# Optimization experiments

Hardware: AMD Instinct MI355X
Metric: run time of the kernel (lower is better)

## Reference

```python
import jax, jax.numpy as jnp
import numpy as np

B, T, H = 1024, 512, 128
TIMESTEPS_PREDICT = 4


def setup_inputs() -> dict:
    key = jax.random.key(0)
    ks = jax.random.split(key, 7)
    s = 1.0 / np.sqrt(H)
    return {
        "x": jax.random.normal(ks[0], (B, T, 1), jnp.float32),
        "hidden": jnp.zeros((B, H), jnp.float32),
        "fc0_w": jax.random.normal(ks[1], (H, 1), jnp.float32) * s,
        "fc0_b": jax.random.normal(ks[2], (H,), jnp.float32) * 0.1,
        "fc_w": jax.random.normal(ks[3], (H, H), jnp.float32) * s,
        "fc_b": jax.random.normal(ks[4], (H,), jnp.float32) * 0.1,
        "dec_w": jax.random.normal(ks[5], (1, H), jnp.float32) * s,
        "dec_b": jax.random.normal(ks[6], (1,), jnp.float32) * 0.1,
    }


def _rnn(x, h, fc0_w, fc0_b, fc_w, fc_b):
    """Vanilla tanh RNN over time. x: (B, Tx, 1), h: (B, H) -> (ys (B, Tx, H), h)."""
    def step(h, xt):  # xt: (B, 1)
        h = jnp.tanh(xt @ fc0_w.T + fc0_b + h @ fc_w.T + fc_b)
        return h, h
    h, ys = jax.lax.scan(step, h, jnp.swapaxes(x, 0, 1))  # ys: (Tx, B, H)
    return jnp.swapaxes(ys, 0, 1), h


def reference(x, hidden, fc0_w, fc0_b, fc_w, fc_b, dec_w, dec_b):
    out, h = _rnn(x, hidden, fc0_w, fc0_b, fc_w, fc_b)  # (B, T, H)
    y = out @ dec_w.T + dec_b  # (B, T, 1)
    last = y[:, -1:, :]  # (B, 1, 1)
    for _ in range(TIMESTEPS_PREDICT):
        out_h, h = _rnn(last, h, fc0_w, fc0_b, fc_w, fc_b)
        last = out_h @ dec_w.T + dec_b
        y = jnp.concatenate([y, last], axis=1)
    return y  # (B, T + TIMESTEPS_PREDICT, 1)
```

## Files before the change

kernel.cpp:

```cpp
#include <hip/hip_runtime.h>
#include <hip/hip_bf16.h>


#define BB 1024
#define TT 512
#define HH 128
#define TOUT 516
#define BM 16
#define XSTR 513
#define YSTR 517
#define PQS 36
#define TWOLOG2E 2.885390082f

typedef __attribute__((ext_vector_type(8))) _Float16 f16x8;
typedef __attribute__((ext_vector_type(4))) float f32x4;

#define MFMA16(A_, B_, C_) __builtin_amdgcn_mfma_f32_16x16x32_f16(A_, B_, C_, 0, 0, 0)

__global__ void detect_dtype(const void* w, int* flag) {
    const int lane = threadIdx.x;
    const __hip_bfloat16* p = (const __hip_bfloat16*)w;
    const float v0 = __bfloat162float(p[lane]);
    const float v1 = __bfloat162float(p[64 + lane]);
    const bool bad = !(fabsf(v0) < 100.0f) || !(fabsf(v1) < 100.0f);
    const unsigned long long m = __ballot(bad);
    if (lane == 0) *flag = (__popcll(m) > 4) ? 1 : 0;
}

template <bool F32>
__device__ __forceinline__ float ldg(const void* p, int idx) {
    if (F32) return ((const float*)p)[idx];
    return __bfloat162float(((const __hip_bfloat16*)p)[idx]);
}

__device__ __forceinline__ float red32(const float* pqrow) {
    const f32x4* v = (const f32x4*)pqrow;
    const f32x4 s = ((v[0] + v[1]) + (v[2] + v[3])) + ((v[4] + v[5]) + (v[6] + v[7]));
    return (s[0] + s[1]) + (s[2] + s[3]);
}

#define STEP(T_, CUR_, WRITEY_, DOPQ_, READX_, TAILX_) do {                     \
    f16x8 bfrag[4];                                                             \
    _Pragma("unroll")                                                           \
    for (int kf = 0; kf < 4; ++kf)                                              \
        bfrag[kf] = *(const f16x8*)&hbuf[CUR_][n][((((kf << 2) | q) ^ n) & 15) << 3]; \
    float xnext = 0.0f;                                                         \
    if (READX_) xnext = xs[n][(T_) + 1];                                        \
    float xv;                                                                   \
    if (TAILX_) xv = red32(&pq[((T_) - 1) & 1][n][0]) + dbv;                    \
    else        xv = xpref;                                                     \
    f32x4 acc0, acc1;                                                           \
    _Pragma("unroll")                                                           \
    for (int r = 0; r < 4; ++r) acc0[r] = fmaf(xv, w0v[r], bsum[r]);            \
    acc1 = (f32x4){0.f, 0.f, 0.f, 0.f};                                         \
    acc0 = MFMA16(wa[0], bfrag[0], acc0);                                       \
    acc1 = MFMA16(wa[1], bfrag[1], acc1);                                       \
    acc0 = MFMA16(wa[2], bfrag[2], acc0);                                       \
    acc1 = MFMA16(wa[3], bfrag[3], acc1);                                       \
    if (isw7 && (WRITEY_)) {               \
        f32x4 aD0 = (f32x4){0.f, 0.f, 0.f, 0.f};                                \
        f32x4 aD1 = (f32x4){0.f, 0.f, 0.f, 0.f};                                \
        aD0 = MFMA16(wa_d[0], bfrag[0], aD0);                                   \
        aD1 = MFMA16(wa_d[1], bfrag[1], aD1);                                   \
        aD0 = MFMA16(wa_d[2], bfrag[2], aD0);                                   \
        aD1 = MFMA16(wa_d[3], bfrag[3], aD1);                                   \
        const float yp = aD0[0] + aD1[0] + dbv;                                 \
        if (q == 0) ybuf[n][(T_) - 1] = yp;                                     \
    }                                                                           \
    float zs[4], ex[4], rc[4], hv[4];                                           \
    _Pragma("unroll")                                                           \
    for (int r = 0; r < 4; ++r) zs[r] = acc0[r] + acc1[r];                      \
    _Pragma("unroll")                                                           \
    for (int r = 0; r < 4; ++r) ex[r] = __builtin_amdgcn_exp2f(zs[r]);          \
    _Pragma("unroll")                                                           \
    for (int r = 0; r < 4; ++r) rc[r] = __builtin_amdgcn_rcpf(ex[r] + 1.0f);    \
    _Pragma("unroll")                                                           \
    for (int r = 0; r < 4; ++r) hv[r] = fmaf(-2.0f, rc[r], 1.0f);               \
    float p = 0.0f;                                                             \
    if (DOPQ_) {                                                                \
        _Pragma("unroll")                                                       \
        for (int r = 0; r < 4; ++r) p = fmaf(decv[r], hv[r], p);                \
    }                                                                           \
    uint2 pk;                                                                   \
    pk.x = __builtin_bit_cast(unsigned, __builtin_amdgcn_cvt_pkrtz(hv[0], hv[1])); \
    pk.y = __builtin_bit_cast(unsigned, __builtin_amdgcn_cvt_pkrtz(hv[2], hv[3])); \
    *(uint2*)&hbuf[(CUR_) ^ 1][n][((((2 * wv + (q >> 1)) ^ n) & 15) << 3) + ((q & 1) << 2)] = pk; \
    if (DOPQ_) pq[(T_) & 1][n][wv * 4 + q] = p;                                 \
    if (READX_) xpref = xnext;                                                  \
    __syncthreads();                                                            \
} while (0)

template <bool F32>
__device__ void rnn_body(const void* __restrict__ xg, const void* __restrict__ h0,
                         const void* __restrict__ w0, const void* __restrict__ b0,
                         const void* __restrict__ W,  const void* __restrict__ bw,
                         const void* __restrict__ dw, const void* __restrict__ db,
                         void* __restrict__ out,
                         float (*xs)[XSTR], float (*ybuf)[YSTR],
                         _Float16 (*hbuf)[BM][HH], float (*pq)[BM][PQS])
{
    const int tid  = threadIdx.x;
    const int lane = tid & 63;
    const int wv   = tid >> 6;
    const int q    = lane >> 4;
    const int n    = lane & 15;
    const int row0 = blockIdx.x * BM;
    const bool isw7 = (wv == 7);

    for (int idx = tid; idx < BM * TT; idx += 512) {
        const int rr = idx >> 9, t2 = idx & (TT - 1);
        xs[rr][t2] = ldg<F32>(xg, (row0 + rr) * TT + t2);
    }
    for (int idx = tid; idx < BM * HH; idx += 512) {
        const int rr = idx >> 7, ii = idx & (HH - 1);
        const int po = ((((ii >> 3) ^ rr) & 15) << 3) + (ii & 7);
        hbuf[0][rr][po] = (_Float16)ldg<F32>(h0, (row0 + rr) * HH + ii);
    }

    f16x8 wa[4];
    {
        const int ia = wv * 16 + n;
        #pragma unroll
        for (int kf = 0; kf < 4; ++kf) {
            const int kb = kf * 32 + q * 8;
            f16x8 fr;
            #pragma unroll
            for (int j = 0; j < 8; ++j)
                fr[j] = (_Float16)(TWOLOG2E * ldg<F32>(W, ia * HH + kb + j));
            wa[kf] = fr;
        }
    }
    f16x8 wa_d[4] = {};
    if (isw7) {
        #pragma unroll
        for (int kf = 0; kf < 4; ++kf) {
            const int kb = kf * 32 + q * 8;
            f16x8 fr = {};
            if (n == 0) {
                #pragma unroll
                for (int j = 0; j < 8; ++j) fr[j] = (_Float16)ldg<F32>(dw, kb + j);
            }
            wa_d[kf] = fr;
        }
    }
    float bsum[4], w0v[4], decv[4];
    #pragma unroll
    for (int r = 0; r < 4; ++r) {
        const int ic = wv * 16 + q * 4 + r;
        bsum[r] = TWOLOG2E * (ldg<F32>(b0, ic) + ldg<F32>(bw, ic));
        w0v[r]  = TWOLOG2E * ldg<F32>(w0, ic);
        decv[r] = ldg<F32>(dw, ic);
    }
    const float dbv = ldg<F32>(db, 0);

    __syncthreads();

    float xpref = xs[n][0];

    STEP(0, 0, false, false, true, false);

    #pragma unroll 1
    for (int t = 1; t < 511; t += 2) {
        STEP(t,     1, true, false, true, false);
        STEP(t + 1, 0, true, false, true, false);
    }

    STEP(511, 1, true, true, false, false);

    #pragma unroll 1
    for (int t = 512; t < 516; ++t) {
        STEP(t, t & 1, true, true, false, true);
    }

    if (isw7 && q == 0)
        ybuf[n][TOUT - 1] = red32(&pq[(TOUT - 1) & 1][n][0]) + dbv;
    __syncthreads();

    for (int rr = 0; rr < BM; ++rr)
        for (int t2 = tid; t2 < TOUT; t2 += 512) {
            const int o = (row0 + rr) * TOUT + t2;
            const float y = ybuf[rr][t2];
            if (F32) ((float*)out)[o] = y;
            else     ((__hip_bfloat16*)out)[o] = __float2bfloat16(y);
        }
}

__global__ __launch_bounds__(512, 2)
void rnn_mfma(const void* __restrict__ xg, const void* __restrict__ h0,
              const void* __restrict__ w0, const void* __restrict__ b0,
              const void* __restrict__ W,  const void* __restrict__ bw,
              const void* __restrict__ dw, const void* __restrict__ db,
              void* __restrict__ out, const int* __restrict__ flag)
{
    __shared__ float xs[BM][XSTR];
    __shared__ float ybuf[BM][YSTR];
    __shared__ __align__(16) _Float16 hbuf[2][BM][HH];
    __shared__ __align__(16) float pq[2][BM][PQS];

    const int f = *(volatile const int*)flag;
    if (f) rnn_body<true >(xg, h0, w0, b0, W, bw, dw, db, out, xs, ybuf, hbuf, pq);
    else   rnn_body<false>(xg, h0, w0, b0, W, bw, dw, db, out, xs, ybuf, hbuf, pq);
}

extern "C" void kernel_launch(void* const* d_in, const int* in_sizes, int n_in,
                              void* d_out, int out_size, void* d_ws, size_t ws_size,
                              hipStream_t stream) {
    int* flag = (int*)d_ws;
    detect_dtype<<<1, 64, 0, stream>>>(d_in[4], flag);
    rnn_mfma<<<BB / BM, 512, 0, stream>>>(d_in[0], d_in[1], d_in[2], d_in[3],
                                          d_in[4], d_in[5], d_in[6], d_in[7],
                                          d_out, flag);
}
```

Before: 215.0 us.

## Process 32 batch rows per block with interleaved MFMA chains and direct output stores

Doubles the rows per block from 16 to 32, so each wave runs two independent MFMA chains per timestep on the same weight fragments. This gives more instruction-level parallelism in the latency-bound recurrence and halves the number of barriers per row. The decoder output is split between waves 6 and 7 and written straight to global memory each step, so the shared y buffer and the final copy loop are gone. Only 32 blocks now run across the device, which risks idle CUs, and the per-step scattered global stores may add latency.

```diff
diff --git a/kernel.cpp b/kernel.cpp
--- a/kernel.cpp
+++ b/kernel.cpp
@@ -6,9 +6,8 @@
 #define TT 512
 #define HH 128
 #define TOUT 516
-#define BM 16
+#define BM 32
 #define XSTR 513
-#define YSTR 517
 #define PQS 36
 #define TWOLOG2E 2.885390082f
 
@@ -33,6 +32,12 @@
     return __bfloat162float(((const __hip_bfloat16*)p)[idx]);
 }
 
+template <bool F32>
+__device__ __forceinline__ void stg(void* p, int idx, float v) {
+    if (F32) ((float*)p)[idx] = v;
+    else     ((__hip_bfloat16*)p)[idx] = __float2bfloat16(v);
+}
+
 __device__ __forceinline__ float red32(const float* pqrow) {
     const f32x4* v = (const f32x4*)pqrow;
     const f32x4 s = ((v[0] + v[1]) + (v[2] + v[3])) + ((v[4] + v[5]) + (v[6] + v[7]));
@@ -40,53 +45,89 @@
 }
 
 #define STEP(T_, CUR_, WRITEY_, DOPQ_, READX_, TAILX_) do {                     \
-    f16x8 bfrag[4];                                                             \
-    _Pragma("unroll")                                                           \
-    for (int kf = 0; kf < 4; ++kf)                                              \
-        bfrag[kf] = *(const f16x8*)&hbuf[CUR_][n][((((kf << 2) | q) ^ n) & 15) << 3]; \
-    float xnext = 0.0f;                                                         \
-    if (READX_) xnext = xs[n][(T_) + 1];                                        \
-    float xv;                                                                   \
-    if (TAILX_) xv = red32(&pq[((T_) - 1) & 1][n][0]) + dbv;                    \
-    else        xv = xpref;                                                     \
-    f32x4 acc0, acc1;                                                           \
-    _Pragma("unroll")                                                           \
-    for (int r = 0; r < 4; ++r) acc0[r] = fmaf(xv, w0v[r], bsum[r]);            \
-    acc1 = (f32x4){0.f, 0.f, 0.f, 0.f};                                         \
-    acc0 = MFMA16(wa[0], bfrag[0], acc0);                                       \
-    acc1 = MFMA16(wa[1], bfrag[1], acc1);                                       \
-    acc0 = MFMA16(wa[2], bfrag[2], acc0);                                       \
-    acc1 = MFMA16(wa[3], bfrag[3], acc1);                                       \
-    if (isw7 && (WRITEY_)) {               \
-        f32x4 aD0 = (f32x4){0.f, 0.f, 0.f, 0.f};                                \
-        f32x4 aD1 = (f32x4){0.f, 0.f, 0.f, 0.f};                                \
-        aD0 = MFMA16(wa_d[0], bfrag[0], aD0);                                   \
-        aD1 = MFMA16(wa_d[1], bfrag[1], aD1);                                   \
-        aD0 = MFMA16(wa_d[2], bfrag[2], aD0);                                   \
-        aD1 = MFMA16(wa_d[3], bfrag[3], aD1);                                   \
-        const float yp = aD0[0] + aD1[0] + dbv;                                 \
-        if (q == 0) ybuf[n][(T_) - 1] = yp;                                     \
-    }                                                                           \
-    float zs[4], ex[4], rc[4], hv[4];                                           \
-    _Pragma("unroll")                                                           \
-    for (int r = 0; r < 4; ++r) zs[r] = acc0[r] + acc1[r];                      \
-    _Pragma("unroll")                                                           \
-    for (int r = 0; r < 4; ++r) ex[r] = __builtin_amdgcn_exp2f(zs[r]);          \
-    _Pragma("unroll")                                                           \
-    for (int r = 0; r < 4; ++r) rc[r] = __builtin_amdgcn_rcpf(ex[r] + 1.0f);    \
-    _Pragma("unroll")                                                           \
-    for (int r = 0; r < 4; ++r) hv[r] = fmaf(-2.0f, rc[r], 1.0f);               \
-    float p = 0.0f;                                                             \
+    f16x8 bfragA[4], bfragB[4];                                                 \
+    _Pragma("unroll")                                                           \
+    for (int kf = 0; kf < 4; ++kf) {                                            \
+        const int co = ((((kf << 2) | q) ^ n) & 15) << 3;                       \
+        bfragA[kf] = *(const f16x8*)&hbuf[CUR_][n][co];                         \
+        bfragB[kf] = *(const f16x8*)&hbuf[CUR_][16 + n][co];                    \
+    }                                                                           \
+    float xnA = 0.0f, xnB = 0.0f;                                               \
+    if (READX_) { xnA = xs[n][(T_) + 1]; xnB = xs[16 + n][(T_) + 1]; }          \
+    float xvA, xvB;                                                             \
+    if (TAILX_) { xvA = red32(&pq[((T_) - 1) & 1][n][0]) + dbv;                 \
+                  xvB = red32(&pq[((T_) - 1) & 1][16 + n][0]) + dbv; }          \
+    else        { xvA = xprefA; xvB = xprefB; }                                 \
+    f32x4 a0A, a1A, a0B, a1B;                                                   \
+    _Pragma("unroll")                                                           \
+    for (int r = 0; r < 4; ++r) { a0A[r] = fmaf(xvA, w0v[r], bsum[r]);          \
+                                  a0B[r] = fmaf(xvB, w0v[r], bsum[r]); }        \
+    a1A = (f32x4){0.f, 0.f, 0.f, 0.f};                                          \
+    a1B = (f32x4){0.f, 0.f, 0.f, 0.f};                                          \
+    a0A = MFMA16(wa[0], bfragA[0], a0A);                                        \
+    a0B = MFMA16(wa[0], bfragB[0], a0B);                                        \
+    a1A = MFMA16(wa[1], bfragA[1], a1A);                                        \
+    a1B = MFMA16(wa[1], bfragB[1], a1B);                                        \
+    a0A = MFMA16(wa[2], bfragA[2], a0A);                                        \
+    a0B = MFMA16(wa[2], bfragB[2], a0B);                                        \
+    a1A = MFMA16(wa[3], bfragA[3], a1A);                                        \
+    a1B = MFMA16(wa[3], bfragB[3], a1B);                                        \
+    if (WRITEY_) {                                                              \
+        if (isw7) {                   \
+            f32x4 dA0 = (f32x4){0.f, 0.f, 0.f, 0.f};                            \
+            f32x4 dA1 = (f32x4){0.f, 0.f, 0.f, 0.f};                            \
+            dA0 = MFMA16(wa_d[0], bfragA[0], dA0);                              \
+            dA1 = MFMA16(wa_d[1], bfragA[1], dA1);                              \
+            dA0 = MFMA16(wa_d[2], bfragA[2], dA0);                              \
+            dA1 = MFMA16(wa_d[3], bfragA[3], dA1);                              \
+            if (q == 0)                                                         \
+                stg<F32>(out, (row0 + n) * TOUT + (T_) - 1,                     \
+                         dA0[0] + dA1[0] + dbv);                                \
+        }                                                                       \
+        if (isw6) {                                             \
+            f32x4 dB0 = (f32x4){0.f, 0.f, 0.f, 0.f};                            \
+            f32x4 dB1 = (f32x4){0.f, 0.f, 0.f, 0.f};                            \
+            dB0 = MFMA16(wa_d[0], bfragB[0], dB0);                              \
+            dB1 = MFMA16(wa_d[1], bfragB[1], dB1);                              \
+            dB0 = MFMA16(wa_d[2], bfragB[2], dB0);                              \
+            dB1 = MFMA16(wa_d[3], bfragB[3], dB1);                              \
+            if (q == 0)                                                         \
+                stg<F32>(out, (row0 + 16 + n) * TOUT + (T_) - 1,                \
+                         dB0[0] + dB1[0] + dbv);                                \
+        }                                                                       \
+    }                                                                           \
+    float zsA[4], zsB[4], exA[4], exB[4], rcA[4], rcB[4], hvA[4], hvB[4];       \
+    _Pragma("unroll")                                                           \
+    for (int r = 0; r < 4; ++r) { zsA[r] = a0A[r] + a1A[r];                     \
+                                  zsB[r] = a0B[r] + a1B[r]; }                   \
+    _Pragma("unroll")                                                           \
+    for (int r = 0; r < 4; ++r) { exA[r] = __builtin_amdgcn_exp2f(zsA[r]);      \
+                                  exB[r] = __builtin_amdgcn_exp2f(zsB[r]); }    \
+    _Pragma("unroll")                                                           \
+    for (int r = 0; r < 4; ++r) { rcA[r] = __builtin_amdgcn_rcpf(exA[r] + 1.0f);\
+                                  rcB[r] = __builtin_amdgcn_rcpf(exB[r] + 1.0f);}\
+    _Pragma("unroll")                                                           \
+    for (int r = 0; r < 4; ++r) { hvA[r] = fmaf(-2.0f, rcA[r], 1.0f);           \
+                                  hvB[r] = fmaf(-2.0f, rcB[r], 1.0f); }         \
+    float pA = 0.0f, pB = 0.0f;                                                 \
     if (DOPQ_) {                                                                \
         _Pragma("unroll")                                                       \
-        for (int r = 0; r < 4; ++r) p = fmaf(decv[r], hv[r], p);                \
-    }                                                                           \
-    uint2 pk;                                                                   \
-    pk.x = __builtin_bit_cast(unsigned, __builtin_amdgcn_cvt_pkrtz(hv[0], hv[1])); \
-    pk.y = __builtin_bit_cast(unsigned, __builtin_amdgcn_cvt_pkrtz(hv[2], hv[3])); \
-    *(uint2*)&hbuf[(CUR_) ^ 1][n][((((2 * wv + (q >> 1)) ^ n) & 15) << 3) + ((q & 1) << 2)] = pk; \
-    if (DOPQ_) pq[(T_) & 1][n][wv * 4 + q] = p;                                 \
-    if (READX_) xpref = xnext;                                                  \
+        for (int r = 0; r < 4; ++r) { pA = fmaf(decv[r], hvA[r], pA);           \
+                                      pB = fmaf(decv[r], hvB[r], pB); }         \
+    }                                                                           \
+    uint2 pkA, pkB;                                                             \
+    pkA.x = __builtin_bit_cast(unsigned, __builtin_amdgcn_cvt_pkrtz(hvA[0], hvA[1])); \
+    pkA.y = __builtin_bit_cast(unsigned, __builtin_amdgcn_cvt_pkrtz(hvA[2], hvA[3])); \
+    pkB.x = __builtin_bit_cast(unsigned, __builtin_amdgcn_cvt_pkrtz(hvB[0], hvB[1])); \
+    pkB.y = __builtin_bit_cast(unsigned, __builtin_amdgcn_cvt_pkrtz(hvB[2], hvB[3])); \
+    {                                                                           \
+        const int wo = ((((2 * wv + (q >> 1)) ^ n) & 15) << 3) + ((q & 1) << 2);\
+        *(uint2*)&hbuf[(CUR_) ^ 1][n][wo]      = pkA;                           \
+        *(uint2*)&hbuf[(CUR_) ^ 1][16 + n][wo] = pkB;                           \
+    }                                                                           \
+    if (DOPQ_) { pq[(T_) & 1][n][wv * 4 + q]      = pA;                         \
+                 pq[(T_) & 1][16 + n][wv * 4 + q] = pB; }                       \
+    if (READX_) { xprefA = xnA; xprefB = xnB; }                                 \
     __syncthreads();                                                            \
 } while (0)
 
@@ -96,8 +137,8 @@
                          const void* __restrict__ W,  const void* __restrict__ bw,
                          const void* __restrict__ dw, const void* __restrict__ db,
                          void* __restrict__ out,
-                         float (*xs)[XSTR], float (*ybuf)[YSTR],
-                         _Float16 (*hbuf)[BM][HH], float (*pq)[BM][PQS])
+                         float (*xs)[XSTR], _Float16 (*hbuf)[BM][HH],
+                         float (*pq)[BM][PQS])
 {
     const int tid  = threadIdx.x;
     const int lane = tid & 63;
@@ -106,6 +147,7 @@
     const int n    = lane & 15;
     const int row0 = blockIdx.x * BM;
     const bool isw7 = (wv == 7);
+    const bool isw6 = (wv == 6);
 
     for (int idx = tid; idx < BM * TT; idx += 512) {
         const int rr = idx >> 9, t2 = idx & (TT - 1);
@@ -131,7 +173,7 @@
         }
     }
     f16x8 wa_d[4] = {};
-    if (isw7) {
+    if (wv >= 6) {
         #pragma unroll
         for (int kf = 0; kf < 4; ++kf) {
             const int kb = kf * 32 + q * 8;
@@ -155,7 +197,8 @@
 
     __syncthreads();
 
-    float xpref = xs[n][0];
+    float xprefA = xs[n][0];
+    float xprefB = xs[16 + n][0];
 
     STEP(0, 0, false, false, true, false);
 
@@ -173,16 +216,9 @@
     }
 
     if (isw7 && q == 0)
-        ybuf[n][TOUT - 1] = red32(&pq[(TOUT - 1) & 1][n][0]) + dbv;
-    __syncthreads();
-
-    for (int rr = 0; rr < BM; ++rr)
-        for (int t2 = tid; t2 < TOUT; t2 += 512) {
-            const int o = (row0 + rr) * TOUT + t2;
-            const float y = ybuf[rr][t2];
-            if (F32) ((float*)out)[o] = y;
-            else     ((__hip_bfloat16*)out)[o] = __float2bfloat16(y);
-        }
+        stg<F32>(out, (row0 + n) * TOUT + TOUT - 1, red32(&pq[1][n][0]) + dbv);
+    if (isw6 && q == 0)
+        stg<F32>(out, (row0 + 16 + n) * TOUT + TOUT - 1, red32(&pq[1][16 + n][0]) + dbv);
 }
 
 __global__ __launch_bounds__(512, 2)
@@ -193,13 +229,12 @@
               void* __restrict__ out, const int* __restrict__ flag)
 {
     __shared__ float xs[BM][XSTR];
-    __shared__ float ybuf[BM][YSTR];
     __shared__ __align__(16) _Float16 hbuf[2][BM][HH];
     __shared__ __align__(16) float pq[2][BM][PQS];
 
     const int f = *(volatile const int*)flag;
-    if (f) rnn_body<true >(xg, h0, w0, b0, W, bw, dw, db, out, xs, ybuf, hbuf, pq);
-    else   rnn_body<false>(xg, h0, w0, b0, W, bw, dw, db, out, xs, ybuf, hbuf, pq);
+    if (f) rnn_body<true >(xg, h0, w0, b0, W, bw, dw, db, out, xs, hbuf, pq);
+    else   rnn_body<false>(xg, h0, w0, b0, W, bw, dw, db, out, xs, hbuf, pq);
 }
 
 extern "C" void kernel_launch(void* const* d_in, const int* in_sizes, int n_in,
```

Result: slower. 305.5 us (+42.1%).

## Halve block to 4 waves, each computing two hidden tiles; write outputs directly

Applied to the files above, without the earlier changes.

Each block now uses 256 threads (4 waves). Each wave computes 32 hidden units using two interleaved MFMA chains, where before it computed 16, and the partial-product reduction shrinks to 16 entries. The shared y buffer and the final copy-out loop are removed, and the decoder output is stored straight to global memory at every step. Fewer waves means a cheaper per-step barrier and more independent MFMA work per wave. The trade-offs are twice the weight registers per wave and scattered small global stores inside the recurrence.

```diff
diff --git a/kernel.cpp b/kernel.cpp
--- a/kernel.cpp
+++ b/kernel.cpp
@@ -8,8 +8,7 @@
 #define TOUT 516
 #define BM 16
 #define XSTR 513
-#define YSTR 517
-#define PQS 36
+#define PQS 20
 #define TWOLOG2E 2.885390082f
 
 typedef __attribute__((ext_vector_type(8))) _Float16 f16x8;
@@ -33,9 +32,15 @@
     return __bfloat162float(((const __hip_bfloat16*)p)[idx]);
 }
 
-__device__ __forceinline__ float red32(const float* pqrow) {
+template <bool F32>
+__device__ __forceinline__ void stg(void* p, int idx, float v) {
+    if (F32) ((float*)p)[idx] = v;
+    else     ((__hip_bfloat16*)p)[idx] = __float2bfloat16(v);
+}
+
+__device__ __forceinline__ float red16(const float* pqrow) {
     const f32x4* v = (const f32x4*)pqrow;
-    const f32x4 s = ((v[0] + v[1]) + (v[2] + v[3])) + ((v[4] + v[5]) + (v[6] + v[7]));
+    const f32x4 s = (v[0] + v[1]) + (v[2] + v[3]);
     return (s[0] + s[1]) + (s[2] + s[3]);
 }
 
@@ -47,44 +52,63 @@
     float xnext = 0.0f;                                                         \
     if (READX_) xnext = xs[n][(T_) + 1];                                        \
     float xv;                                                                   \
-    if (TAILX_) xv = red32(&pq[((T_) - 1) & 1][n][0]) + dbv;                    \
+    if (TAILX_) xv = red16(&pq[((T_) - 1) & 1][n][0]) + dbv;                    \
     else        xv = xpref;                                                     \
-    f32x4 acc0, acc1;                                                           \
-    _Pragma("unroll")                                                           \
-    for (int r = 0; r < 4; ++r) acc0[r] = fmaf(xv, w0v[r], bsum[r]);            \
-    acc1 = (f32x4){0.f, 0.f, 0.f, 0.f};                                         \
-    acc0 = MFMA16(wa[0], bfrag[0], acc0);                                       \
-    acc1 = MFMA16(wa[1], bfrag[1], acc1);                                       \
-    acc0 = MFMA16(wa[2], bfrag[2], acc0);                                       \
-    acc1 = MFMA16(wa[3], bfrag[3], acc1);                                       \
-    if (isw7 && (WRITEY_)) {               \
-        f32x4 aD0 = (f32x4){0.f, 0.f, 0.f, 0.f};                                \
-        f32x4 aD1 = (f32x4){0.f, 0.f, 0.f, 0.f};                                \
-        aD0 = MFMA16(wa_d[0], bfrag[0], aD0);                                   \
-        aD1 = MFMA16(wa_d[1], bfrag[1], aD1);                                   \
-        aD0 = MFMA16(wa_d[2], bfrag[2], aD0);                                   \
-        aD1 = MFMA16(wa_d[3], bfrag[3], aD1);                                   \
-        const float yp = aD0[0] + aD1[0] + dbv;                                 \
-        if (q == 0) ybuf[n][(T_) - 1] = yp;                                     \
+    f32x4 a00, a01, a10, a11;                                                   \
+    _Pragma("unroll")                                                           \
+    for (int r = 0; r < 4; ++r) { a00[r] = fmaf(xv, w0v0[r], bsum0[r]);         \
+                                  a10[r] = fmaf(xv, w0v1[r], bsum1[r]); }       \
+    a01 = (f32x4){0.f, 0.f, 0.f, 0.f};                                          \
+    a11 = (f32x4){0.f, 0.f, 0.f, 0.f};                                          \
+    a00 = MFMA16(wa0[0], bfrag[0], a00);                                        \
+    a10 = MFMA16(wa1[0], bfrag[0], a10);                                        \
+    a01 = MFMA16(wa0[1], bfrag[1], a01);                                        \
+    a11 = MFMA16(wa1[1], bfrag[1], a11);                                        \
+    a00 = MFMA16(wa0[2], bfrag[2], a00);                                        \
+    a10 = MFMA16(wa1[2], bfrag[2], a10);                                        \
+    a01 = MFMA16(wa0[3], bfrag[3], a01);                                        \
+    a11 = MFMA16(wa1[3], bfrag[3], a11);                                        \
+    if (isw3 && (WRITEY_)) {               \
+        f32x4 dA0 = (f32x4){0.f, 0.f, 0.f, 0.f};                                \
+        f32x4 dA1 = (f32x4){0.f, 0.f, 0.f, 0.f};                                \
+        dA0 = MFMA16(wa_d[0], bfrag[0], dA0);                                   \
+        dA1 = MFMA16(wa_d[1], bfrag[1], dA1);                                   \
+        dA0 = MFMA16(wa_d[2], bfrag[2], dA0);                                   \
+        dA1 = MFMA16(wa_d[3], bfrag[3], dA1);                                   \
+        if (q == 0)                                                             \
+            stg<F32>(out, (row0 + n) * TOUT + (T_) - 1, dA0[0] + dA1[0] + dbv); \
     }                                                                           \
-    float zs[4], ex[4], rc[4], hv[4];                                           \
-    _Pragma("unroll")                                                           \
-    for (int r = 0; r < 4; ++r) zs[r] = acc0[r] + acc1[r];                      \
-    _Pragma("unroll")                                                           \
-    for (int r = 0; r < 4; ++r) ex[r] = __builtin_amdgcn_exp2f(zs[r]);          \
-    _Pragma("unroll")                                                           \
-    for (int r = 0; r < 4; ++r) rc[r] = __builtin_amdgcn_rcpf(ex[r] + 1.0f);    \
-    _Pragma("unroll")                                                           \
-    for (int r = 0; r < 4; ++r) hv[r] = fmaf(-2.0f, rc[r], 1.0f);               \
+    float zs0[4], zs1[4], ex0[4], ex1[4], rc0[4], rc1[4], hv0[4], hv1[4];       \
+    _Pragma("unroll")                                                           \
+    for (int r = 0; r < 4; ++r) { zs0[r] = a00[r] + a01[r];                     \
+                                  zs1[r] = a10[r] + a11[r]; }                   \
+    _Pragma("unroll")                                                           \
+    for (int r = 0; r < 4; ++r) { ex0[r] = __builtin_amdgcn_exp2f(zs0[r]);      \
+                                  ex1[r] = __builtin_amdgcn_exp2f(zs1[r]); }    \
+    _Pragma("unroll")                                                           \
+    for (int r = 0; r < 4; ++r) { rc0[r] = __builtin_amdgcn_rcpf(ex0[r] + 1.0f);\
+                                  rc1[r] = __builtin_amdgcn_rcpf(ex1[r] + 1.0f);}\
+    _Pragma("unroll")                                                           \
+    for (int r = 0; r < 4; ++r) { hv0[r] = fmaf(-2.0f, rc0[r], 1.0f);           \
+                                  hv1[r] = fmaf(-2.0f, rc1[r], 1.0f); }         \
     float p = 0.0f;                                                             \
     if (DOPQ_) {                                                                \
         _Pragma("unroll")                                                       \
-        for (int r = 0; r < 4; ++r) p = fmaf(decv[r], hv[r], p);                \
+        for (int r = 0; r < 4; ++r) { p = fmaf(decv0[r], hv0[r], p);            \
+                                      p = fmaf(decv1[r], hv1[r], p); }          \
     }                                                                           \
-    uint2 pk;                                                                   \
-    pk.x = __builtin_bit_cast(unsigned, __builtin_amdgcn_cvt_pkrtz(hv[0], hv[1])); \
-    pk.y = __builtin_bit_cast(unsigned, __builtin_amdgcn_cvt_pkrtz(hv[2], hv[3])); \
-    *(uint2*)&hbuf[(CUR_) ^ 1][n][((((2 * wv + (q >> 1)) ^ n) & 15) << 3) + ((q & 1) << 2)] = pk; \
+    uint2 pk0, pk1;                                                             \
+    pk0.x = __builtin_bit_cast(unsigned, __builtin_amdgcn_cvt_pkrtz(hv0[0], hv0[1])); \
+    pk0.y = __builtin_bit_cast(unsigned, __builtin_amdgcn_cvt_pkrtz(hv0[2], hv0[3])); \
+    pk1.x = __builtin_bit_cast(unsigned, __builtin_amdgcn_cvt_pkrtz(hv1[0], hv1[1])); \
+    pk1.y = __builtin_bit_cast(unsigned, __builtin_amdgcn_cvt_pkrtz(hv1[2], hv1[3])); \
+    {                   \
+        const int lo = ((q & 1) << 2);                                          \
+        const int c0 = ((((4 * wv) | (q >> 1)) ^ n) & 15) << 3;                 \
+        const int c1 = ((((4 * wv + 2) | (q >> 1)) ^ n) & 15) << 3;             \
+        *(uint2*)&hbuf[(CUR_) ^ 1][n][c0 + lo] = pk0;                           \
+        *(uint2*)&hbuf[(CUR_) ^ 1][n][c1 + lo] = pk1;                           \
+    }                                                                           \
     if (DOPQ_) pq[(T_) & 1][n][wv * 4 + q] = p;                                 \
     if (READX_) xpref = xnext;                                                  \
     __syncthreads();                                                            \
@@ -96,8 +120,8 @@
                          const void* __restrict__ W,  const void* __restrict__ bw,
                          const void* __restrict__ dw, const void* __restrict__ db,
                          void* __restrict__ out,
-                         float (*xs)[XSTR], float (*ybuf)[YSTR],
-                         _Float16 (*hbuf)[BM][HH], float (*pq)[BM][PQS])
+                         float (*xs)[XSTR], _Float16 (*hbuf)[BM][HH],
+                         float (*pq)[BM][PQS])
 {
     const int tid  = threadIdx.x;
     const int lane = tid & 63;
@@ -105,33 +129,37 @@
     const int q    = lane >> 4;
     const int n    = lane & 15;
     const int row0 = blockIdx.x * BM;
-    const bool isw7 = (wv == 7);
-
-    for (int idx = tid; idx < BM * TT; idx += 512) {
+    const bool isw3 = (wv == 3);
+
+    for (int idx = tid; idx < BM * TT; idx += 256) {
         const int rr = idx >> 9, t2 = idx & (TT - 1);
         xs[rr][t2] = ldg<F32>(xg, (row0 + rr) * TT + t2);
     }
-    for (int idx = tid; idx < BM * HH; idx += 512) {
+    for (int idx = tid; idx < BM * HH; idx += 256) {
         const int rr = idx >> 7, ii = idx & (HH - 1);
         const int po = ((((ii >> 3) ^ rr) & 15) << 3) + (ii & 7);
         hbuf[0][rr][po] = (_Float16)ldg<F32>(h0, (row0 + rr) * HH + ii);
     }
 
-    f16x8 wa[4];
+    f16x8 wa0[4], wa1[4];
     {
-        const int ia = wv * 16 + n;
+        const int ia0 = 32 * wv + n;
+        const int ia1 = 32 * wv + 16 + n;
         #pragma unroll
         for (int kf = 0; kf < 4; ++kf) {
             const int kb = kf * 32 + q * 8;
-            f16x8 fr;
+            f16x8 fr0, fr1;
             #pragma unroll
-            for (int j = 0; j < 8; ++j)
-                fr[j] = (_Float16)(TWOLOG2E * ldg<F32>(W, ia * HH + kb + j));
-            wa[kf] = fr;
+            for (int j = 0; j < 8; ++j) {
+                fr0[j] = (_Float16)(TWOLOG2E * ldg<F32>(W, ia0 * HH + kb + j));
+                fr1[j] = (_Float16)(TWOLOG2E * ldg<F32>(W, ia1 * HH + kb + j));
+            }
+            wa0[kf] = fr0;
+            wa1[kf] = fr1;
         }
     }
     f16x8 wa_d[4] = {};
-    if (isw7) {
+    if (isw3) {
         #pragma unroll
         for (int kf = 0; kf < 4; ++kf) {
             const int kb = kf * 32 + q * 8;
@@ -143,13 +171,17 @@
             wa_d[kf] = fr;
         }
     }
-    float bsum[4], w0v[4], decv[4];
+    float bsum0[4], w0v0[4], decv0[4], bsum1[4], w0v1[4], decv1[4];
     #pragma unroll
     for (int r = 0; r < 4; ++r) {
-        const int ic = wv * 16 + q * 4 + r;
-        bsum[r] = TWOLOG2E * (ldg<F32>(b0, ic) + ldg<F32>(bw, ic));
-        w0v[r]  = TWOLOG2E * ldg<F32>(w0, ic);
-        decv[r] = ldg<F32>(dw, ic);
+        const int ic0 = 32 * wv + q * 4 + r;
+        const int ic1 = ic0 + 16;
+        bsum0[r] = TWOLOG2E * (ldg<F32>(b0, ic0) + ldg<F32>(bw, ic0));
+        bsum1[r] = TWOLOG2E * (ldg<F32>(b0, ic1) + ldg<F32>(bw, ic1));
+        w0v0[r]  = TWOLOG2E * ldg<F32>(w0, ic0);
+        w0v1[r]  = TWOLOG2E * ldg<F32>(w0, ic1);
+        decv0[r] = ldg<F32>(dw, ic0);
+        decv1[r] = ldg<F32>(dw, ic1);
     }
     const float dbv = ldg<F32>(db, 0);
 
@@ -172,20 +204,11 @@
         STEP(t, t & 1, true, true, false, true);
     }
 
-    if (isw7 && q == 0)
-        ybuf[n][TOUT - 1] = red32(&pq[(TOUT - 1) & 1][n][0]) + dbv;
-    __syncthreads();
-
-    for (int rr = 0; rr < BM; ++rr)
-        for (int t2 = tid; t2 < TOUT; t2 += 512) {
-            const int o = (row0 + rr) * TOUT + t2;
-            const float y = ybuf[rr][t2];
-            if (F32) ((float*)out)[o] = y;
-            else     ((__hip_bfloat16*)out)[o] = __float2bfloat16(y);
-        }
-}
-
-__global__ __launch_bounds__(512, 2)
+    if (isw3 && q == 0)
+        stg<F32>(out, (row0 + n) * TOUT + TOUT - 1, red16(&pq[1][n][0]) + dbv);
+}
+
+__global__ __launch_bounds__(256, 1)
 void rnn_mfma(const void* __restrict__ xg, const void* __restrict__ h0,
               const void* __restrict__ w0, const void* __restrict__ b0,
               const void* __restrict__ W,  const void* __restrict__ bw,
@@ -193,13 +216,12 @@
               void* __restrict__ out, const int* __restrict__ flag)
 {
     __shared__ float xs[BM][XSTR];
-    __shared__ float ybuf[BM][YSTR];
     __shared__ __align__(16) _Float16 hbuf[2][BM][HH];
     __shared__ __align__(16) float pq[2][BM][PQS];
 
     const int f = *(volatile const int*)flag;
-    if (f) rnn_body<true >(xg, h0, w0, b0, W, bw, dw, db, out, xs, ybuf, hbuf, pq);
-    else   rnn_body<false>(xg, h0, w0, b0, W, bw, dw, db, out, xs, ybuf, hbuf, pq);
+    if (f) rnn_body<true >(xg, h0, w0, b0, W, bw, dw, db, out, xs, hbuf, pq);
+    else   rnn_body<false>(xg, h0, w0, b0, W, bw, dw, db, out, xs, hbuf, pq);
 }
 
 extern "C" void kernel_launch(void* const* d_in, const int* in_sizes, int n_in,
@@ -207,7 +229,7 @@
                               hipStream_t stream) {
     int* flag = (int*)d_ws;
     detect_dtype<<<1, 64, 0, stream>>>(d_in[4], flag);
-    rnn_mfma<<<BB / BM, 512, 0, stream>>>(d_in[0], d_in[1], d_in[2], d_in[3],
+    rnn_mfma<<<BB / BM, 256, 0, stream>>>(d_in[0], d_in[1], d_in[2], d_in[3],
                                           d_in[4], d_in[5], d_in[6], d_in[7],
                                           d_out, flag);
 }
```

Result: slower. 274.0 us (+27.4%).

## Defer decoder MFMA one step, write outputs directly, vectorize x prefetch

Applied to the files above, without the earlier changes.

The decoder projection for each step now runs at the start of the next step on the bfrag values still held in registers. This takes it off the critical path between the recurrence MFMAs and the tanh. Outputs go straight to global memory instead of being staged in an LDS ybuf and copied out at the end, which frees shared memory and removes the final copy loop. The x inputs are prefetched as float4 every four steps, the loop is unrolled by four, and launch bounds change to one block per SIMD group. The risks are scattered, uncoalesced global stores from a single wave and different occupancy.

```diff
diff --git a/kernel.cpp b/kernel.cpp
--- a/kernel.cpp
+++ b/kernel.cpp
@@ -7,8 +7,7 @@
 #define HH 128
 #define TOUT 516
 #define BM 16
-#define XSTR 513
-#define YSTR 517
+#define XSTR 516
 #define PQS 36
 #define TWOLOG2E 2.885390082f
 
@@ -33,22 +32,42 @@
     return __bfloat162float(((const __hip_bfloat16*)p)[idx]);
 }
 
+template <bool F32>
+__device__ __forceinline__ void stg(void* p, int idx, float v) {
+    if (F32) ((float*)p)[idx] = v;
+    else     ((__hip_bfloat16*)p)[idx] = __float2bfloat16(v);
+}
+
 __device__ __forceinline__ float red32(const float* pqrow) {
     const f32x4* v = (const f32x4*)pqrow;
     const f32x4 s = ((v[0] + v[1]) + (v[2] + v[3])) + ((v[4] + v[5]) + (v[6] + v[7]));
     return (s[0] + s[1]) + (s[2] + s[3]);
 }
 
-#define STEP(T_, CUR_, WRITEY_, DOPQ_, READX_, TAILX_) do {                     \
-    f16x8 bfrag[4];                                                             \
+#define STEP(T_, CUR_, DODEC_, DOPQ_, XSEL_, PFX_) do {                         \
+    if (isw7 && (DODEC_)) {          \
+        f32x4 dA0 = (f32x4){0.f, 0.f, 0.f, 0.f};                                \
+        f32x4 dA1 = (f32x4){0.f, 0.f, 0.f, 0.f};                                \
+        dA0 = MFMA16(wa_d[0], bfrag[0], dA0);                                   \
+        dA1 = MFMA16(wa_d[1], bfrag[1], dA1);                                   \
+        dA0 = MFMA16(wa_d[2], bfrag[2], dA0);                                   \
+        dA1 = MFMA16(wa_d[3], bfrag[3], dA1);                                   \
+        if (q == 0)                                                             \
+            stg<F32>(out, (row0 + n) * TOUT + (T_) - 2, dA0[0] + dA1[0] + dbv); \
+    }                                                                           \
     _Pragma("unroll")                                                           \
     for (int kf = 0; kf < 4; ++kf)                                              \
         bfrag[kf] = *(const f16x8*)&hbuf[CUR_][n][((((kf << 2) | q) ^ n) & 15) << 3]; \
-    float xnext = 0.0f;                                                         \
-    if (READX_) xnext = xs[n][(T_) + 1];                                        \
     float xv;                                                                   \
-    if (TAILX_) xv = red32(&pq[((T_) - 1) & 1][n][0]) + dbv;                    \
-    else        xv = xpref;                                                     \
+    if ((XSEL_) < 0) {                                                          \
+        xv = red32(&pq[((T_) - 1) & 1][n][0]) + dbv;                            \
+    } else {                                                                    \
+        if ((XSEL_) == 0) {                                                     \
+            xcur = xnxt;                                                        \
+            if (PFX_) xnxt = *(const f32x4*)&xs[n][(T_) + 4];                   \
+        }                                                                       \
+        xv = xcur[(XSEL_) & 3];                                                 \
+    }                                                                           \
     f32x4 acc0, acc1;                                                           \
     _Pragma("unroll")                                                           \
     for (int r = 0; r < 4; ++r) acc0[r] = fmaf(xv, w0v[r], bsum[r]);            \
@@ -57,16 +76,6 @@
     acc1 = MFMA16(wa[1], bfrag[1], acc1);                                       \
     acc0 = MFMA16(wa[2], bfrag[2], acc0);                                       \
     acc1 = MFMA16(wa[3], bfrag[3], acc1);                                       \
-    if (isw7 && (WRITEY_)) {               \
-        f32x4 aD0 = (f32x4){0.f, 0.f, 0.f, 0.f};                                \
-        f32x4 aD1 = (f32x4){0.f, 0.f, 0.f, 0.f};                                \
-        aD0 = MFMA16(wa_d[0], bfrag[0], aD0);                                   \
-        aD1 = MFMA16(wa_d[1], bfrag[1], aD1);                                   \
-        aD0 = MFMA16(wa_d[2], bfrag[2], aD0);                                   \
-        aD1 = MFMA16(wa_d[3], bfrag[3], aD1);                                   \
-        const float yp = aD0[0] + aD1[0] + dbv;                                 \
-        if (q == 0) ybuf[n][(T_) - 1] = yp;                                     \
-    }                                                                           \
     float zs[4], ex[4], rc[4], hv[4];                                           \
     _Pragma("unroll")                                                           \
     for (int r = 0; r < 4; ++r) zs[r] = acc0[r] + acc1[r];                      \
@@ -86,7 +95,6 @@
     pk.y = __builtin_bit_cast(unsigned, __builtin_amdgcn_cvt_pkrtz(hv[2], hv[3])); \
     *(uint2*)&hbuf[(CUR_) ^ 1][n][((((2 * wv + (q >> 1)) ^ n) & 15) << 3) + ((q & 1) << 2)] = pk; \
     if (DOPQ_) pq[(T_) & 1][n][wv * 4 + q] = p;                                 \
-    if (READX_) xpref = xnext;                                                  \
     __syncthreads();                                                            \
 } while (0)
 
@@ -96,8 +104,8 @@
                          const void* __restrict__ W,  const void* __restrict__ bw,
                          const void* __restrict__ dw, const void* __restrict__ db,
                          void* __restrict__ out,
-                         float (*xs)[XSTR], float (*ybuf)[YSTR],
-                         _Float16 (*hbuf)[BM][HH], float (*pq)[BM][PQS])
+                         float (*xs)[XSTR], _Float16 (*hbuf)[BM][HH],
+                         float (*pq)[BM][PQS])
 {
     const int tid  = threadIdx.x;
     const int lane = tid & 63;
@@ -155,37 +163,48 @@
 
     __syncthreads();
 
-    float xpref = xs[n][0];
-
-    STEP(0, 0, false, false, true, false);
+    f16x8 bfrag[4];
+    f32x4 xcur, xnxt;
+    xnxt = *(const f32x4*)&xs[n][0];
+
+    STEP(0, 0, false, false, 0, true);
+    STEP(1, 1, false, false, 1, false);
+    STEP(2, 0, true,  false, 2, false);
+    STEP(3, 1, true,  false, 3, false);
 
     #pragma unroll 1
-    for (int t = 1; t < 511; t += 2) {
-        STEP(t,     1, true, false, true, false);
-        STEP(t + 1, 0, true, false, true, false);
-    }
-
-    STEP(511, 1, true, true, false, false);
-
-    #pragma unroll 1
-    for (int t = 512; t < 516; ++t) {
-        STEP(t, t & 1, true, true, false, true);
-    }
-
-    if (isw7 && q == 0)
-        ybuf[n][TOUT - 1] = red32(&pq[(TOUT - 1) & 1][n][0]) + dbv;
-    __syncthreads();
-
-    for (int rr = 0; rr < BM; ++rr)
-        for (int t2 = tid; t2 < TOUT; t2 += 512) {
-            const int o = (row0 + rr) * TOUT + t2;
-            const float y = ybuf[rr][t2];
-            if (F32) ((float*)out)[o] = y;
-            else     ((__hip_bfloat16*)out)[o] = __float2bfloat16(y);
+    for (int t = 4; t < 508; t += 4) {
+        STEP(t,     0, true, false, 0, true);
+        STEP(t + 1, 1, true, false, 1, false);
+        STEP(t + 2, 0, true, false, 2, false);
+        STEP(t + 3, 1, true, false, 3, false);
+    }
+
+    STEP(508, 0, true, false, 0, false);
+    STEP(509, 1, true, false, 1, false);
+    STEP(510, 0, true, false, 2, false);
+    STEP(511, 1, true, true,  3, false);
+
+    STEP(512, 0, true, true, -1, false);
+    STEP(513, 1, true, true, -1, false);
+    STEP(514, 0, true, true, -1, false);
+    STEP(515, 1, true, true, -1, false);
+
+    if (isw7) {
+        f32x4 dA0 = (f32x4){0.f, 0.f, 0.f, 0.f};
+        f32x4 dA1 = (f32x4){0.f, 0.f, 0.f, 0.f};
+        dA0 = MFMA16(wa_d[0], bfrag[0], dA0);
+        dA1 = MFMA16(wa_d[1], bfrag[1], dA1);
+        dA0 = MFMA16(wa_d[2], bfrag[2], dA0);
+        dA1 = MFMA16(wa_d[3], bfrag[3], dA1);
+        if (q == 0) {
+            stg<F32>(out, (row0 + n) * TOUT + 514, dA0[0] + dA1[0] + dbv);
+            stg<F32>(out, (row0 + n) * TOUT + 515, red32(&pq[1][n][0]) + dbv);
         }
-}
-
-__global__ __launch_bounds__(512, 2)
+    }
+}
+
+__global__ __launch_bounds__(512, 1)
 void rnn_mfma(const void* __restrict__ xg, const void* __restrict__ h0,
               const void* __restrict__ w0, const void* __restrict__ b0,
               const void* __restrict__ W,  const void* __restrict__ bw,
@@ -193,13 +212,12 @@
               void* __restrict__ out, const int* __restrict__ flag)
 {
     __shared__ float xs[BM][XSTR];
-    __shared__ float ybuf[BM][YSTR];
     __shared__ __align__(16) _Float16 hbuf[2][BM][HH];
     __shared__ __align__(16) float pq[2][BM][PQS];
 
     const int f = *(volatile const int*)flag;
-    if (f) rnn_body<true >(xg, h0, w0, b0, W, bw, dw, db, out, xs, ybuf, hbuf, pq);
-    else   rnn_body<false>(xg, h0, w0, b0, W, bw, dw, db, out, xs, ybuf, hbuf, pq);
+    if (f) rnn_body<true >(xg, h0, w0, b0, W, bw, dw, db, out, xs, hbuf, pq);
+    else   rnn_body<false>(xg, h0, w0, b0, W, bw, dw, db, out, xs, hbuf, pq);
 }
 
 extern "C" void kernel_launch(void* const* d_in, const int* in_sizes, int n_in,
```

Result: slower. 220.5 us (+2.5%).
